# Kernel optimization log

Measured on AMD Instinct MI355X. Metric: run time of the kernel, lower is better.

The kernel has to match this reference:

```python
import jax, jax.numpy as jnp
import numpy as np

H = 8          # num_heads
T = 2          # num_edge_types
NEG_SLOPE = 0.2


def _edge_softmax(scores, dst, num_nodes):
    # softmax over incoming edges of each destination node, per head
    m = jax.ops.segment_max(scores, dst, num_segments=num_nodes)  # [N,H]
    e = jnp.exp(scores - m[dst])                                   # [E,H]
    s = jax.ops.segment_sum(e, dst, num_segments=num_nodes)        # [N,H]
    return e / s[dst]


def setup_inputs() -> dict:
    key = jax.random.key(0)
    ks = jax.random.split(key, 8)
    N, D, E = 50000, 128, 800000
    return {
        "x": jax.random.normal(ks[0], (N, D), dtype=jnp.float32),
        "w_u": jax.random.normal(ks[1], (H * T, D), dtype=jnp.float32) * (1.0 / np.sqrt(D)),
        "b_u": jax.random.normal(ks[2], (H * T,), dtype=jnp.float32) * 0.01,
        "w_v": jax.random.normal(ks[3], (H * T, D), dtype=jnp.float32) * (1.0 / np.sqrt(D)),
        "src_e0": jax.random.randint(ks[4], (E,), 0, N, dtype=jnp.int32),
        "dst_e0": jax.random.randint(ks[5], (E,), 0, N, dtype=jnp.int32),
        "src_e1": jax.random.randint(ks[6], (E,), 0, N, dtype=jnp.int32),
        "dst_e1": jax.random.randint(ks[7], (E,), 0, N, dtype=jnp.int32),
    }


def reference(x, w_u, b_u, w_v, src_e0, dst_e0, src_e1, dst_e1):
    N, D = x.shape
    head_dim = D // H
    scores_u = x @ w_u.T + b_u   # [N, H*T]
    scores_v = x @ w_v.T         # [N, H*T]
    xh = x.reshape(N, head_dim, H)  # matches torch reshape(-1, head_dim, num_heads)
    outs = [x]  # sep=True
    for t, (src, dst) in enumerate([(src_e0, dst_e0), (src_e1, dst_e1)]):
        u = scores_u[:, t * H:(t + 1) * H]
        v = scores_v[:, t * H:(t + 1) * H]
        s = u[src] + v[dst]                         # u_add_v -> [E,H]
        s = jnp.where(s >= 0, s, NEG_SLOPE * s)     # LeakyReLU(0.2)
        p = _edge_softmax(s, dst, N)                # [E,H]
        msg = xh[src] * p[:, None, :]               # u_mul_e -> [E,head_dim,H]
        agg = jax.ops.segment_sum(msg, dst, num_segments=N)  # [N,head_dim,H]
        outs.append(agg.reshape(N, D))
    return jnp.concatenate(outs, axis=-1)  # [N, D*(1+T)]
```

## Files before the change

### kernel.cpp

```cpp
#include <hip/hip_runtime.h>

#define NEG_SLOPE 0.2f
#define CHUNKP 2048
#define RSHIFT 11
#define RW     2048
#define MAXR   32

__device__ __forceinline__ ushort f2bf(float f) {
    union { float f; unsigned u; } c; c.f = f;
    unsigned u = c.u;
    return (ushort)((u + 0x7fffu + ((u >> 16) & 1u)) >> 16);
}

__global__ __launch_bounds__(256) void mega_kernel(
    const float* __restrict__ x, const float* __restrict__ wu,
    const float* __restrict__ bu, const float* __restrict__ wv,
    const int* __restrict__ s0, const int* __restrict__ d0,
    const int* __restrict__ s1, const int* __restrict__ d1,
    float* __restrict__ out, ushort* __restrict__ xbf,
    float* __restrict__ su, float* __restrict__ sv,
    int* __restrict__ gcur, unsigned* __restrict__ pairs,
    int N, int E, int nr, int cap, int convBlocks, int scoreBlocks, int ppset)
{
    __shared__ float wlds[32 * 129];
    __shared__ int lcnt[MAXR], gb[MAXR], lrun[MAXR];
    int tid = threadIdx.x;
    int bid = blockIdx.x;

    if (bid < convBlocks) {
        int i = bid * 256 + tid;
        if (i < N * 32) {
            float4 v = ((const float4*)x)[i];
            int n = i >> 5, q = i & 31;
            ((float4*)out)[(size_t)n * 96 + q] = v;
            ushort4 b;
            b.x = f2bf(v.x); b.y = f2bf(v.y); b.z = f2bf(v.z); b.w = f2bf(v.w);
            *(ushort4*)(xbf + (size_t)i * 4) = b;
        }
        return;
    }
    if (bid < convBlocks + scoreBlocks) {
        for (int i = tid; i < 4096; i += 256) {
            int o = i >> 7, k = i & 127;
            wlds[o * 129 + k] = (o < 16) ? wu[i] : wv[i - 2048];
        }
        __syncthreads();
        int o = tid & 15;
        int n = (bid - convBlocks) * 16 + (tid >> 4);
        if (n >= N) return;
        const float4* xr4 = (const float4*)(x + (size_t)n * 128);
        const float* wur = wlds + o * 129;
        const float* wvr = wlds + (16 + o) * 129;
        float au = 0.f, av = 0.f;
#pragma unroll
        for (int kk = 0; kk < 32; ++kk) {
            float4 xv = xr4[kk];
            int k = kk * 4;
            au = fmaf(xv.x, wur[k],     au);  av = fmaf(xv.x, wvr[k],     av);
            au = fmaf(xv.y, wur[k + 1], au);  av = fmaf(xv.y, wvr[k + 1], av);
            au = fmaf(xv.z, wur[k + 2], au);  av = fmaf(xv.z, wvr[k + 2], av);
            au = fmaf(xv.w, wur[k + 3], au);  av = fmaf(xv.w, wvr[k + 3], av);
        }
        su[n * 16 + o] = au + bu[o];
        sv[n * 16 + o] = av;
        return;
    }
    int pb = bid - convBlocks - scoreBlocks;
    int t = pb / ppset, c = pb % ppset;
    const int* ss = t ? s1 : s0;
    const int* dd = t ? d1 : d0;
    int beg = c * CHUNKP, end = min(E, beg + CHUNKP);
    if (tid < nr) lcnt[tid] = 0;
    __syncthreads();
    for (int e = beg + tid; e < end; e += 256)
        atomicAdd(&lcnt[dd[e] >> RSHIFT], 1);
    __syncthreads();
    if (tid < nr) {
        gb[tid] = atomicAdd(&gcur[t * MAXR + tid], lcnt[tid]);
        lrun[tid] = 0;
    }
    __syncthreads();
    unsigned* pt = pairs + (size_t)t * nr * cap;
    for (int e = beg + tid; e < end; e += 256) {
        int dst = dd[e], src = ss[e];
        int r = dst >> RSHIFT;
        int pos = atomicAdd(&lrun[r], 1);
        pt[(size_t)r * cap + gb[r] + pos] = ((unsigned)dst << 16) | (unsigned)src;
    }
}

__global__ __launch_bounds__(1024) void build_kernel(
    const unsigned* __restrict__ pairs, const int* __restrict__ gcur,
    int* __restrict__ off, ushort* __restrict__ bucket,
    int N, int E, int nr, int cap)
{
    __shared__ int hist[RW];
    __shared__ int lds[1024];
    int r = blockIdx.x, t = blockIdx.y, tid = threadIdx.x;
    int m = gcur[t * MAXR + r];
    int base = 0;
    if (tid < 32) {
        int v = (tid < r) ? gcur[t * MAXR + tid] : 0;
#pragma unroll
        for (int d = 1; d < 32; d <<= 1) v += __shfl_xor(v, d);
        if (tid == 0) lds[0] = v;
    }
    hist[tid] = 0; hist[tid + 1024] = 0;
    __syncthreads();
    base = lds[0];
    __syncthreads();
    const unsigned* p = pairs + ((size_t)t * nr + r) * cap;
    for (int i = tid; i < m; i += 1024)
        atomicAdd(&hist[(p[i] >> 16) & (RW - 1)], 1);
    __syncthreads();
    int h0 = hist[2 * tid], h1 = hist[2 * tid + 1];
    int tot = h0 + h1;
    lds[tid] = tot;
    __syncthreads();
    int incl = tot;
    for (int d = 1; d < 1024; d <<= 1) {
        int add = (tid >= d) ? lds[tid - d] : 0;
        __syncthreads();
        incl += add;
        lds[tid] = incl;
        __syncthreads();
    }
    int e0 = incl - tot, e1 = incl - tot + h0;
    int lo = r << RSHIFT;
    int* offt = off + (size_t)t * (N + 1);
    if (lo + 2 * tid < N)     offt[lo + 2 * tid]     = base + e0;
    if (lo + 2 * tid + 1 < N) offt[lo + 2 * tid + 1] = base + e1;
    hist[2 * tid] = e0; hist[2 * tid + 1] = e1;
    if (r == 0 && tid == 0) offt[N] = E;
    __syncthreads();
    ushort* bkt = bucket + (size_t)t * E + base;
    for (int i = tid; i < m; i += 1024) {
        unsigned v = p[i];
        int pos = atomicAdd(&hist[(v >> 16) & (RW - 1)], 1);
        bkt[pos] = (ushort)(v & 0xffffu);
    }
}

__global__ __launch_bounds__(256) void agg_kernel(
    const ushort* __restrict__ xbf, const float* __restrict__ su,
    const float* __restrict__ sv, const int* __restrict__ off,
    const ushort* __restrict__ bucket, float* __restrict__ out, int N, int E)
{
    __shared__ __align__(16) float evals[4][512];
    int t = blockIdx.y;
    int wid = threadIdx.x >> 6;
    int lane = threadIdx.x & 63;
    int n = blockIdx.x * 4 + wid;
    if (n >= N) return;
    const int* offt = off + (size_t)t * (N + 1);
    const ushort* bkt = bucket + (size_t)t * E;
    int beg = offt[n], end = offt[n + 1];
    int h = lane & 7;
    int e8 = lane >> 3;
    float vh = sv[n * 16 + t * 8 + h];
    float* ev = evals[wid];

    int hf = lane >> 5;
    int q = lane & 31;
    int j0 = q * 4;
    int hbase = (q & 1) * 4;
    float acc0 = 0.f, acc1 = 0.f, acc2 = 0.f, acc3 = 0.f;
    float l = 0.f;

    for (int cbeg = beg; cbeg < end; cbeg += 64) {
        int cnt = min(end - cbeg, 64);
        int gmax = (cnt + 7) >> 3;
        for (int g = 0; g < gmax; ++g) {
            int e = g * 8 + e8;
            bool valid = e < cnt;
            int srcv = 0;
            if (valid) srcv = bkt[cbeg + e];
            float s = su[srcv * 16 + t * 8 + h] + vh;
            s = (s >= 0.f) ? s : NEG_SLOPE * s;
            float eval = valid ? __expf(s) : 0.f;
            l += eval;
            ev[e * 8 + h] = eval;
        }
        int pairs2 = (cnt + 1) >> 1;
        for (int i2 = 0; i2 < pairs2; ++i2) {
            int eidx = i2 * 2 + hf;
            int srcv = 0;
            if (eidx < cnt) srcv = bkt[cbeg + eidx];
            float4 p4 = *(const float4*)(ev + eidx * 8 + hbase);
            uint2 u = *(const uint2*)(xbf + (size_t)srcv * 128 + j0);
            float x0 = __uint_as_float(u.x << 16);
            float x1 = __uint_as_float(u.x & 0xffff0000u);
            float x2 = __uint_as_float(u.y << 16);
            float x3 = __uint_as_float(u.y & 0xffff0000u);
            acc0 = fmaf(x0, p4.x, acc0);
            acc1 = fmaf(x1, p4.y, acc1);
            acc2 = fmaf(x2, p4.z, acc2);
            acc3 = fmaf(x3, p4.w, acc3);
        }
    }
    l += __shfl_xor(l, 8);
    l += __shfl_xor(l, 16);
    l += __shfl_xor(l, 32);
    float invl = (l > 0.f) ? (1.f / l) : 0.f;
    acc0 += __shfl_xor(acc0, 32);
    acc1 += __shfl_xor(acc1, 32);
    acc2 += __shfl_xor(acc2, 32);
    acc3 += __shfl_xor(acc3, 32);
    float i0 = __shfl(invl, hbase);
    float i1 = __shfl(invl, hbase + 1);
    float i2v = __shfl(invl, hbase + 2);
    float i3 = __shfl(invl, hbase + 3);
    if (hf == 0) {
        float4 r = make_float4(acc0 * i0, acc1 * i1, acc2 * i2v, acc3 * i3);
        *(float4*)(out + (size_t)n * 384 + 128 + (size_t)t * 128 + j0) = r;
    }
}

extern "C" void kernel_launch(void* const* d_in, const int* in_sizes, int n_in,
                              void* d_out, int out_size, void* d_ws, size_t ws_size,
                              hipStream_t stream)
{
    const float* x  = (const float*)d_in[0];
    const float* wu = (const float*)d_in[1];
    const float* bu = (const float*)d_in[2];
    const float* wv = (const float*)d_in[3];
    const int* s0 = (const int*)d_in[4];
    const int* d0 = (const int*)d_in[5];
    const int* s1 = (const int*)d_in[6];
    const int* d1 = (const int*)d_in[7];
    float* out = (float*)d_out;
    int N = in_sizes[0] / 128;
    int E = in_sizes[4];

    int nr = ((N - 1) >> RSHIFT) + 1;
    long long mean = (long long)RW * E / N;
    int cap = (int)(mean + mean / 4 + 2048);

    char* ws = (char*)d_ws;
    size_t o = 0;
    auto alloc = [&](size_t bytes) -> void* {
        void* p = ws + o;
        o = (o + bytes + 255) & ~(size_t)255;
        return p;
    };
    float* su       = (float*)alloc((size_t)N * 16 * 4);
    float* sv       = (float*)alloc((size_t)N * 16 * 4);
    int* gcur       = (int*)alloc((size_t)2 * MAXR * 4);
    int* off        = (int*)alloc((size_t)2 * (N + 1) * 4);
    unsigned* pairs = (unsigned*)alloc((size_t)2 * nr * cap * 4);
    ushort* bucket  = (ushort*)alloc((size_t)2 * E * 2);
    ushort* xbf     = (ushort*)alloc((size_t)N * 128 * 2);

    int convBlocks  = (N * 32 + 255) / 256;
    int scoreBlocks = (N + 15) / 16;
    int ppset       = (E + CHUNKP - 1) / CHUNKP;

    hipMemsetAsync(gcur, 0, (size_t)2 * MAXR * 4, stream);
    mega_kernel<<<convBlocks + scoreBlocks + 2 * ppset, 256, 0, stream>>>(
        x, wu, bu, wv, s0, d0, s1, d1, out, xbf, su, sv,
        gcur, pairs, N, E, nr, cap, convBlocks, scoreBlocks, ppset);
    build_kernel<<<dim3(nr, 2), 1024, 0, stream>>>(
        pairs, gcur, off, bucket, N, E, nr, cap);
    agg_kernel<<<dim3((N + 3) / 4, 2), 256, 0, stream>>>(
        xbf, su, sv, off, bucket, out, N, E);
}
```

Measured before the change: 273.4 us.

## Fuse all stages into one persistent cooperative kernel with grid syncs

Replaces the memset and the three separate kernel launches with a single cooperative persistent kernel. Grid-wide syncs separate the conversion/score, partition, CSR build and aggregation phases, and blocks loop over work items. The destination-range width shrinks from 2048 to 512 nodes, so there are more, smaller build items that fit 256-thread blocks, and per-block work is coarsened. This removes launch gaps and memset overhead. In exchange, grid barriers become a cost, and the persistent grid is sized by occupancy, which may limit parallelism in the aggregation phase.

New measurement: 1.064 ms. +289.0%, slower.

```diff
diff --git a/kernel.cpp b/kernel.cpp
--- a/kernel.cpp
+++ b/kernel.cpp
@@ -1,10 +1,12 @@
 #include <hip/hip_runtime.h>
+#include <hip/hip_cooperative_groups.h>
+
+namespace cg = cooperative_groups;
 
 #define NEG_SLOPE 0.2f
+#define RSHIFT 9
+#define RW     512
 #define CHUNKP 2048
-#define RSHIFT 11
-#define RW     2048
-#define MAXR   32
 
 __device__ __forceinline__ ushort f2bf(float f) {
     union { float f; unsigned u; } c; c.f = f;
@@ -12,7 +14,7 @@
     return (ushort)((u + 0x7fffu + ((u >> 16) & 1u)) >> 16);
 }
 
-__global__ __launch_bounds__(256) void mega_kernel(
+__global__ __launch_bounds__(256, 8) void fused_kernel(
     const float* __restrict__ x, const float* __restrict__ wu,
     const float* __restrict__ bu, const float* __restrict__ wv,
     const int* __restrict__ s0, const int* __restrict__ d0,
@@ -20,199 +22,208 @@
     float* __restrict__ out, ushort* __restrict__ xbf,
     float* __restrict__ su, float* __restrict__ sv,
     int* __restrict__ gcur, unsigned* __restrict__ pairs,
-    int N, int E, int nr, int cap, int convBlocks, int scoreBlocks, int ppset)
+    ushort* __restrict__ bucket, int* __restrict__ off,
+    int N, int E, int nr, int cap,
+    int convItems, int scoreItems, int partItems, int buildItems, int aggItems)
 {
-    __shared__ float wlds[32 * 129];
-    __shared__ int lcnt[MAXR], gb[MAXR], lrun[MAXR];
-    int tid = threadIdx.x;
-    int bid = blockIdx.x;
-
-    if (bid < convBlocks) {
-        int i = bid * 256 + tid;
-        if (i < N * 32) {
-            float4 v = ((const float4*)x)[i];
-            int n = i >> 5, q = i & 31;
-            ((float4*)out)[(size_t)n * 96 + q] = v;
-            ushort4 b;
-            b.x = f2bf(v.x); b.y = f2bf(v.y); b.z = f2bf(v.z); b.w = f2bf(v.w);
-            *(ushort4*)(xbf + (size_t)i * 4) = b;
-        }
-        return;
-    }
-    if (bid < convBlocks + scoreBlocks) {
-        for (int i = tid; i < 4096; i += 256) {
-            int o = i >> 7, k = i & 127;
-            wlds[o * 129 + k] = (o < 16) ? wu[i] : wv[i - 2048];
-        }
-        __syncthreads();
-        int o = tid & 15;
-        int n = (bid - convBlocks) * 16 + (tid >> 4);
-        if (n >= N) return;
-        const float4* xr4 = (const float4*)(x + (size_t)n * 128);
-        const float* wur = wlds + o * 129;
-        const float* wvr = wlds + (16 + o) * 129;
-        float au = 0.f, av = 0.f;
+    cg::grid_group grid = cg::this_grid();
+    __shared__ __align__(16) float smem[4224];
+    __shared__ int misc[8];
+    int* smi = (int*)smem;
+    const int tid = threadIdx.x;
+    const int nb = gridDim.x;
+    const int bid = blockIdx.x;
+
+    if (bid == 0) for (int i = tid; i < 2 * nr; i += 256) gcur[i] = 0;
+    int a1 = convItems + scoreItems;
+    for (int v = bid; v < a1; v += nb) {
+        if (v < convItems) {
+            int base = v * 2048 + tid;
 #pragma unroll
-        for (int kk = 0; kk < 32; ++kk) {
-            float4 xv = xr4[kk];
-            int k = kk * 4;
-            au = fmaf(xv.x, wur[k],     au);  av = fmaf(xv.x, wvr[k],     av);
-            au = fmaf(xv.y, wur[k + 1], au);  av = fmaf(xv.y, wvr[k + 1], av);
-            au = fmaf(xv.z, wur[k + 2], au);  av = fmaf(xv.z, wvr[k + 2], av);
-            au = fmaf(xv.w, wur[k + 3], au);  av = fmaf(xv.w, wvr[k + 3], av);
-        }
-        su[n * 16 + o] = au + bu[o];
-        sv[n * 16 + o] = av;
-        return;
-    }
-    int pb = bid - convBlocks - scoreBlocks;
-    int t = pb / ppset, c = pb % ppset;
-    const int* ss = t ? s1 : s0;
-    const int* dd = t ? d1 : d0;
-    int beg = c * CHUNKP, end = min(E, beg + CHUNKP);
-    if (tid < nr) lcnt[tid] = 0;
-    __syncthreads();
-    for (int e = beg + tid; e < end; e += 256)
-        atomicAdd(&lcnt[dd[e] >> RSHIFT], 1);
-    __syncthreads();
-    if (tid < nr) {
-        gb[tid] = atomicAdd(&gcur[t * MAXR + tid], lcnt[tid]);
-        lrun[tid] = 0;
-    }
-    __syncthreads();
-    unsigned* pt = pairs + (size_t)t * nr * cap;
-    for (int e = beg + tid; e < end; e += 256) {
-        int dst = dd[e], src = ss[e];
-        int r = dst >> RSHIFT;
-        int pos = atomicAdd(&lrun[r], 1);
-        pt[(size_t)r * cap + gb[r] + pos] = ((unsigned)dst << 16) | (unsigned)src;
-    }
-}
-
-__global__ __launch_bounds__(1024) void build_kernel(
-    const unsigned* __restrict__ pairs, const int* __restrict__ gcur,
-    int* __restrict__ off, ushort* __restrict__ bucket,
-    int N, int E, int nr, int cap)
-{
-    __shared__ int hist[RW];
-    __shared__ int lds[1024];
-    int r = blockIdx.x, t = blockIdx.y, tid = threadIdx.x;
-    int m = gcur[t * MAXR + r];
-    int base = 0;
-    if (tid < 32) {
-        int v = (tid < r) ? gcur[t * MAXR + tid] : 0;
+            for (int j = 0; j < 8; ++j) {
+                int i = base + j * 256;
+                if (i < N * 32) {
+                    float4 val = ((const float4*)x)[i];
+                    int n = i >> 5, q = i & 31;
+                    ((float4*)out)[(size_t)n * 96 + q] = val;
+                    ushort4 b;
+                    b.x = f2bf(val.x); b.y = f2bf(val.y);
+                    b.z = f2bf(val.z); b.w = f2bf(val.w);
+                    *(ushort4*)(xbf + (size_t)i * 4) = b;
+                }
+            }
+        } else {
+            int nbase = (v - convItems) * 128;
+            for (int i = tid; i < 4096; i += 256) {
+                int o = i >> 7, k = i & 127;
+                smem[o * 132 + k] = (o < 16) ? wu[i] : wv[i - 2048];
+            }
+            __syncthreads();
+            int o = tid & 15;
+            const float* wur = smem + o * 132;
+            const float* wvr = smem + (16 + o) * 132;
+            for (int sub = 0; sub < 8; ++sub) {
+                int n = nbase + sub * 16 + (tid >> 4);
+                if (n < N) {
+                    const float4* xr4 = (const float4*)(x + (size_t)n * 128);
+                    float au = 0.f, av = 0.f;
 #pragma unroll
-        for (int d = 1; d < 32; d <<= 1) v += __shfl_xor(v, d);
-        if (tid == 0) lds[0] = v;
-    }
-    hist[tid] = 0; hist[tid + 1024] = 0;
-    __syncthreads();
-    base = lds[0];
-    __syncthreads();
-    const unsigned* p = pairs + ((size_t)t * nr + r) * cap;
-    for (int i = tid; i < m; i += 1024)
-        atomicAdd(&hist[(p[i] >> 16) & (RW - 1)], 1);
-    __syncthreads();
-    int h0 = hist[2 * tid], h1 = hist[2 * tid + 1];
-    int tot = h0 + h1;
-    lds[tid] = tot;
-    __syncthreads();
-    int incl = tot;
-    for (int d = 1; d < 1024; d <<= 1) {
-        int add = (tid >= d) ? lds[tid - d] : 0;
-        __syncthreads();
-        incl += add;
-        lds[tid] = incl;
-        __syncthreads();
-    }
-    int e0 = incl - tot, e1 = incl - tot + h0;
-    int lo = r << RSHIFT;
-    int* offt = off + (size_t)t * (N + 1);
-    if (lo + 2 * tid < N)     offt[lo + 2 * tid]     = base + e0;
-    if (lo + 2 * tid + 1 < N) offt[lo + 2 * tid + 1] = base + e1;
-    hist[2 * tid] = e0; hist[2 * tid + 1] = e1;
-    if (r == 0 && tid == 0) offt[N] = E;
-    __syncthreads();
-    ushort* bkt = bucket + (size_t)t * E + base;
-    for (int i = tid; i < m; i += 1024) {
-        unsigned v = p[i];
-        int pos = atomicAdd(&hist[(v >> 16) & (RW - 1)], 1);
-        bkt[pos] = (ushort)(v & 0xffffu);
-    }
-}
-
-__global__ __launch_bounds__(256) void agg_kernel(
-    const ushort* __restrict__ xbf, const float* __restrict__ su,
-    const float* __restrict__ sv, const int* __restrict__ off,
-    const ushort* __restrict__ bucket, float* __restrict__ out, int N, int E)
-{
-    __shared__ __align__(16) float evals[4][512];
-    int t = blockIdx.y;
-    int wid = threadIdx.x >> 6;
-    int lane = threadIdx.x & 63;
-    int n = blockIdx.x * 4 + wid;
-    if (n >= N) return;
-    const int* offt = off + (size_t)t * (N + 1);
-    const ushort* bkt = bucket + (size_t)t * E;
-    int beg = offt[n], end = offt[n + 1];
-    int h = lane & 7;
-    int e8 = lane >> 3;
-    float vh = sv[n * 16 + t * 8 + h];
-    float* ev = evals[wid];
-
-    int hf = lane >> 5;
-    int q = lane & 31;
-    int j0 = q * 4;
-    int hbase = (q & 1) * 4;
-    float acc0 = 0.f, acc1 = 0.f, acc2 = 0.f, acc3 = 0.f;
-    float l = 0.f;
-
-    for (int cbeg = beg; cbeg < end; cbeg += 64) {
-        int cnt = min(end - cbeg, 64);
-        int gmax = (cnt + 7) >> 3;
-        for (int g = 0; g < gmax; ++g) {
-            int e = g * 8 + e8;
-            bool valid = e < cnt;
-            int srcv = 0;
-            if (valid) srcv = bkt[cbeg + e];
-            float s = su[srcv * 16 + t * 8 + h] + vh;
-            s = (s >= 0.f) ? s : NEG_SLOPE * s;
-            float eval = valid ? __expf(s) : 0.f;
-            l += eval;
-            ev[e * 8 + h] = eval;
-        }
-        int pairs2 = (cnt + 1) >> 1;
-        for (int i2 = 0; i2 < pairs2; ++i2) {
-            int eidx = i2 * 2 + hf;
-            int srcv = 0;
-            if (eidx < cnt) srcv = bkt[cbeg + eidx];
-            float4 p4 = *(const float4*)(ev + eidx * 8 + hbase);
-            uint2 u = *(const uint2*)(xbf + (size_t)srcv * 128 + j0);
-            float x0 = __uint_as_float(u.x << 16);
-            float x1 = __uint_as_float(u.x & 0xffff0000u);
-            float x2 = __uint_as_float(u.y << 16);
-            float x3 = __uint_as_float(u.y & 0xffff0000u);
-            acc0 = fmaf(x0, p4.x, acc0);
-            acc1 = fmaf(x1, p4.y, acc1);
-            acc2 = fmaf(x2, p4.z, acc2);
-            acc3 = fmaf(x3, p4.w, acc3);
-        }
-    }
-    l += __shfl_xor(l, 8);
-    l += __shfl_xor(l, 16);
-    l += __shfl_xor(l, 32);
-    float invl = (l > 0.f) ? (1.f / l) : 0.f;
-    acc0 += __shfl_xor(acc0, 32);
-    acc1 += __shfl_xor(acc1, 32);
-    acc2 += __shfl_xor(acc2, 32);
-    acc3 += __shfl_xor(acc3, 32);
-    float i0 = __shfl(invl, hbase);
-    float i1 = __shfl(invl, hbase + 1);
-    float i2v = __shfl(invl, hbase + 2);
-    float i3 = __shfl(invl, hbase + 3);
-    if (hf == 0) {
-        float4 r = make_float4(acc0 * i0, acc1 * i1, acc2 * i2v, acc3 * i3);
-        *(float4*)(out + (size_t)n * 384 + 128 + (size_t)t * 128 + j0) = r;
+                    for (int kk = 0; kk < 32; ++kk) {
+                        float4 xv = xr4[kk];
+                        float4 a4 = *(const float4*)(wur + kk * 4);
+                        float4 b4 = *(const float4*)(wvr + kk * 4);
+                        au = fmaf(xv.x, a4.x, au);  av = fmaf(xv.x, b4.x, av);
+                        au = fmaf(xv.y, a4.y, au);  av = fmaf(xv.y, b4.y, av);
+                        au = fmaf(xv.z, a4.z, au);  av = fmaf(xv.z, b4.z, av);
+                        au = fmaf(xv.w, a4.w, au);  av = fmaf(xv.w, b4.w, av);
+                    }
+                    su[n * 16 + o] = au + bu[o];
+                    sv[n * 16 + o] = av;
+                }
+            }
+            __syncthreads();
+        }
+    }
+    __threadfence();
+    grid.sync();
+
+    int ppset = partItems >> 1;
+    for (int v = bid; v < partItems; v += nb) {
+        int t = v / ppset, c = v % ppset;
+        const int* ss = t ? s1 : s0;
+        const int* dd = t ? d1 : d0;
+        int beg = c * CHUNKP, end = min(E, beg + CHUNKP);
+        int* lcnt = smi; int* gb = smi + 128; int* lrun = smi + 256;
+        if (tid < nr) lcnt[tid] = 0;
+        __syncthreads();
+        for (int e = beg + tid; e < end; e += 256)
+            atomicAdd(&lcnt[dd[e] >> RSHIFT], 1);
+        __syncthreads();
+        if (tid < nr) {
+            gb[tid] = atomicAdd(&gcur[t * nr + tid], lcnt[tid]);
+            lrun[tid] = 0;
+        }
+        __syncthreads();
+        unsigned* pt = pairs + (size_t)t * nr * cap;
+        for (int e = beg + tid; e < end; e += 256) {
+            int dst = dd[e], src = ss[e];
+            int r = dst >> RSHIFT;
+            int pos = atomicAdd(&lrun[r], 1);
+            pt[(size_t)r * cap + gb[r] + pos] = ((unsigned)dst << 16) | (unsigned)src;
+        }
+        __syncthreads();
+    }
+    __threadfence();
+    grid.sync();
+
+    for (int v = bid; v < buildItems; v += nb) {
+        int r = v % nr, t = v / nr;
+        int m = gcur[t * nr + r];
+        int s = (tid < r) ? gcur[t * nr + tid] : 0;
+#pragma unroll
+        for (int d = 1; d < 64; d <<= 1) s += __shfl_xor(s, d);
+        if ((tid & 63) == 0) misc[tid >> 6] = s;
+        int* hist = smi; int* scanb = smi + 512;
+        hist[2 * tid] = 0; hist[2 * tid + 1] = 0;
+        __syncthreads();
+        int base = misc[0] + misc[1] + misc[2] + misc[3];
+        const unsigned* p = pairs + ((size_t)t * nr + r) * cap;
+        for (int i = tid; i < m; i += 256)
+            atomicAdd(&hist[(p[i] >> 16) & (RW - 1)], 1);
+        __syncthreads();
+        int h0 = hist[2 * tid], h1 = hist[2 * tid + 1], tot = h0 + h1;
+        scanb[tid] = tot;
+        __syncthreads();
+        int incl = tot;
+        for (int d = 1; d < 256; d <<= 1) {
+            int add = (tid >= d) ? scanb[tid - d] : 0;
+            __syncthreads();
+            incl += add; scanb[tid] = incl;
+            __syncthreads();
+        }
+        int e0 = incl - tot, e1 = e0 + h0;
+        int lo = r << RSHIFT;
+        int* offt = off + (size_t)t * (N + 1);
+        if (lo + 2 * tid < N)     offt[lo + 2 * tid]     = base + e0;
+        if (lo + 2 * tid + 1 < N) offt[lo + 2 * tid + 1] = base + e1;
+        hist[2 * tid] = e0; hist[2 * tid + 1] = e1;
+        if (r == 0 && tid == 0) offt[N] = E;
+        __syncthreads();
+        ushort* bkt = bucket + (size_t)t * E + base;
+        for (int i = tid; i < m; i += 256) {
+            unsigned pv = p[i];
+            int pos = atomicAdd(&hist[(pv >> 16) & (RW - 1)], 1);
+            bkt[pos] = (ushort)(pv & 0xffffu);
+        }
+        __syncthreads();
+    }
+    __threadfence();
+    grid.sync();
+
+    {
+        int wid = tid >> 6, lane = tid & 63;
+        int h = lane & 7, e8 = lane >> 3;
+        int hf = lane >> 5, q = lane & 31;
+        int j0 = q * 4, hbase = (q & 1) * 4;
+        float* ev = smem + wid * 512;
+        for (int v = bid; v < aggItems; v += nb) {
+            int t = v & 1, gnode = v >> 1;
+            int n = gnode * 4 + wid;
+            if (n >= N) continue;
+            const int* offt = off + (size_t)t * (N + 1);
+            const ushort* bkt = bucket + (size_t)t * E;
+            int beg = offt[n], end = offt[n + 1];
+            float vh = sv[n * 16 + t * 8 + h];
+            float acc0 = 0.f, acc1 = 0.f, acc2 = 0.f, acc3 = 0.f;
+            float l = 0.f;
+            for (int cbeg = beg; cbeg < end; cbeg += 64) {
+                int cnt = min(end - cbeg, 64);
+                int gmax = (cnt + 7) >> 3;
+                for (int g = 0; g < gmax; ++g) {
+                    int e = g * 8 + e8;
+                    bool valid = e < cnt;
+                    int srcv = 0;
+                    if (valid) srcv = bkt[cbeg + e];
+                    float sc = su[srcv * 16 + t * 8 + h] + vh;
+                    sc = (sc >= 0.f) ? sc : NEG_SLOPE * sc;
+                    float eval = valid ? __expf(sc) : 0.f;
+                    l += eval;
+                    ev[e * 8 + h] = eval;
+                }
+                int pairs2 = (cnt + 1) >> 1;
+                for (int i2 = 0; i2 < pairs2; ++i2) {
+                    int eidx = i2 * 2 + hf;
+                    int srcv = 0;
+                    if (eidx < cnt) srcv = bkt[cbeg + eidx];
+                    float4 p4 = *(const float4*)(ev + eidx * 8 + hbase);
+                    uint2 u = *(const uint2*)(xbf + (size_t)srcv * 128 + j0);
+                    float x0 = __uint_as_float(u.x << 16);
+                    float x1 = __uint_as_float(u.x & 0xffff0000u);
+                    float x2 = __uint_as_float(u.y << 16);
+                    float x3 = __uint_as_float(u.y & 0xffff0000u);
+                    acc0 = fmaf(x0, p4.x, acc0);
+                    acc1 = fmaf(x1, p4.y, acc1);
+                    acc2 = fmaf(x2, p4.z, acc2);
+                    acc3 = fmaf(x3, p4.w, acc3);
+                }
+            }
+            l += __shfl_xor(l, 8);
+            l += __shfl_xor(l, 16);
+            l += __shfl_xor(l, 32);
+            float invl = (l > 0.f) ? (1.f / l) : 0.f;
+            acc0 += __shfl_xor(acc0, 32);
+            acc1 += __shfl_xor(acc1, 32);
+            acc2 += __shfl_xor(acc2, 32);
+            acc3 += __shfl_xor(acc3, 32);
+            float i0 = __shfl(invl, hbase);
+            float i1 = __shfl(invl, hbase + 1);
+            float i2v = __shfl(invl, hbase + 2);
+            float i3 = __shfl(invl, hbase + 3);
+            if (hf == 0) {
+                float4 r4 = make_float4(acc0 * i0, acc1 * i1, acc2 * i2v, acc3 * i3);
+                *(float4*)(out + (size_t)n * 384 + 128 + (size_t)t * 128 + j0) = r4;
+            }
+        }
     }
 }
 
@@ -234,7 +245,7 @@
 
     int nr = ((N - 1) >> RSHIFT) + 1;
     long long mean = (long long)RW * E / N;
-    int cap = (int)(mean + mean / 4 + 2048);
+    int cap = (int)(mean + mean / 4 + 1024);
 
     char* ws = (char*)d_ws;
     size_t o = 0;
@@ -245,22 +256,39 @@
     };
     float* su       = (float*)alloc((size_t)N * 16 * 4);
     float* sv       = (float*)alloc((size_t)N * 16 * 4);
-    int* gcur       = (int*)alloc((size_t)2 * MAXR * 4);
+    int* gcur       = (int*)alloc((size_t)2 * nr * 4);
     int* off        = (int*)alloc((size_t)2 * (N + 1) * 4);
     unsigned* pairs = (unsigned*)alloc((size_t)2 * nr * cap * 4);
     ushort* bucket  = (ushort*)alloc((size_t)2 * E * 2);
     ushort* xbf     = (ushort*)alloc((size_t)N * 128 * 2);
 
-    int convBlocks  = (N * 32 + 255) / 256;
-    int scoreBlocks = (N + 15) / 16;
-    int ppset       = (E + CHUNKP - 1) / CHUNKP;
-
-    hipMemsetAsync(gcur, 0, (size_t)2 * MAXR * 4, stream);
-    mega_kernel<<<convBlocks + scoreBlocks + 2 * ppset, 256, 0, stream>>>(
-        x, wu, bu, wv, s0, d0, s1, d1, out, xbf, su, sv,
-        gcur, pairs, N, E, nr, cap, convBlocks, scoreBlocks, ppset);
-    build_kernel<<<dim3(nr, 2), 1024, 0, stream>>>(
-        pairs, gcur, off, bucket, N, E, nr, cap);
-    agg_kernel<<<dim3((N + 3) / 4, 2), 256, 0, stream>>>(
-        xbf, su, sv, off, bucket, out, N, E);
+    int convItems  = (N * 32 + 2047) / 2048;
+    int scoreItems = (N + 127) / 128;
+    int partItems  = 2 * ((E + CHUNKP - 1) / CHUNKP);
+    int buildItems = 2 * nr;
+    int aggItems   = 2 * ((N + 3) / 4);
+
+    int dev = 0;
+    hipGetDevice(&dev);
+    int numCU = 0;
+    hipDeviceGetAttribute(&numCU, hipDeviceAttributeMultiprocessorCount, dev);
+    if (numCU <= 0) numCU = 256;
+    int maxB = 0;
+    hipOccupancyMaxActiveBlocksPerMultiprocessor(&maxB, fused_kernel, 256, 0);
+    if (maxB < 1) maxB = 1;
+    if (maxB > 8) maxB = 8;
+    int nb = numCU * maxB;
+    if (nb > 4096) nb = 4096;
+
+    void* args[] = {
+        (void*)&x, (void*)&wu, (void*)&bu, (void*)&wv,
+        (void*)&s0, (void*)&d0, (void*)&s1, (void*)&d1,
+        (void*)&out, (void*)&xbf, (void*)&su, (void*)&sv,
+        (void*)&gcur, (void*)&pairs, (void*)&bucket, (void*)&off,
+        (void*)&N, (void*)&E, (void*)&nr, (void*)&cap,
+        (void*)&convItems, (void*)&scoreItems, (void*)&partItems,
+        (void*)&buildItems, (void*)&aggItems
+    };
+    hipLaunchCooperativeKernel((const void*)fused_kernel, dim3(nb), dim3(256),
+                               args, 0, stream);
 }
```

## Fuse CSR build into aggregation using 64-node buckets sorted in LDS

Applied to the files above, without the earlier changes.

Destination regions shrink from 2048 nodes to 64 nodes. Each block of the new fused kernel now counting-sorts its region's packed (dst,src) pairs in shared memory and then aggregates the softmax-weighted messages directly. This removes the global offset and bucket arrays, one kernel launch, and the global round trip of the sorted source indices. In exchange, the partition kernel maintains far more per-chunk counters (up to 800, kept in reused LDS), and each wave processes 16 nodes in sequence. Per-region counts are clamped to a fixed capacity, so an unusually heavy region would silently drop edges.

After: 261.8 us. 4.3% less time.

```diff
diff --git a/kernel.cpp b/kernel.cpp
--- a/kernel.cpp
+++ b/kernel.cpp
@@ -1,10 +1,10 @@
 #include <hip/hip_runtime.h>
 
 #define NEG_SLOPE 0.2f
-#define CHUNKP 2048
-#define RSHIFT 11
-#define RW     2048
-#define MAXR   32
+#define RSHIFT 6
+#define RW     64
+#define MAXNR  800
+#define CHUNKP 8192
 
 __device__ __forceinline__ ushort f2bf(float f) {
     union { float f; unsigned u; } c; c.f = f;
@@ -23,7 +23,7 @@
     int N, int E, int nr, int cap, int convBlocks, int scoreBlocks, int ppset)
 {
     __shared__ float wlds[32 * 129];
-    __shared__ int lcnt[MAXR], gb[MAXR], lrun[MAXR];
+    int* smi = (int*)wlds;
     int tid = threadIdx.x;
     int bid = blockIdx.x;
 
@@ -70,14 +70,15 @@
     const int* ss = t ? s1 : s0;
     const int* dd = t ? d1 : d0;
     int beg = c * CHUNKP, end = min(E, beg + CHUNKP);
-    if (tid < nr) lcnt[tid] = 0;
+    int* lcnt = smi; int* gb = smi + MAXNR; int* lrun = smi + 2 * MAXNR;
+    for (int i = tid; i < nr; i += 256) lcnt[i] = 0;
     __syncthreads();
     for (int e = beg + tid; e < end; e += 256)
         atomicAdd(&lcnt[dd[e] >> RSHIFT], 1);
     __syncthreads();
-    if (tid < nr) {
-        gb[tid] = atomicAdd(&gcur[t * MAXR + tid], lcnt[tid]);
-        lrun[tid] = 0;
+    for (int i = tid; i < nr; i += 256) {
+        gb[i] = atomicAdd(&gcur[t * nr + i], lcnt[i]);
+        lrun[i] = 0;
     }
     __syncthreads();
     unsigned* pt = pairs + (size_t)t * nr * cap;
@@ -89,130 +90,103 @@
     }
 }
 
-__global__ __launch_bounds__(1024) void build_kernel(
-    const unsigned* __restrict__ pairs, const int* __restrict__ gcur,
-    int* __restrict__ off, ushort* __restrict__ bucket,
+__global__ __launch_bounds__(256, 8) void buildagg_kernel(
+    const ushort* __restrict__ xbf, const float* __restrict__ su,
+    const float* __restrict__ sv, const int* __restrict__ gcur,
+    const unsigned* __restrict__ pairs, float* __restrict__ out,
     int N, int E, int nr, int cap)
 {
-    __shared__ int hist[RW];
-    __shared__ int lds[1024];
+    __shared__ ushort srcs[1408];
+    __shared__ int offl[65];
+    __shared__ int cursor[64];
+    __shared__ __align__(16) float ev4[4][512];
     int r = blockIdx.x, t = blockIdx.y, tid = threadIdx.x;
-    int m = gcur[t * MAXR + r];
-    int base = 0;
-    if (tid < 32) {
-        int v = (tid < r) ? gcur[t * MAXR + tid] : 0;
+    int m = gcur[t * nr + r];
+    if (m > cap) m = cap;
+    const unsigned* p = pairs + ((size_t)t * nr + r) * cap;
+
+    if (tid < 64) cursor[tid] = 0;
+    __syncthreads();
+    for (int i = tid; i < m; i += 256)
+        atomicAdd(&cursor[(p[i] >> 16) & (RW - 1)], 1);
+    __syncthreads();
+    if (tid < 64) {
+        int v = cursor[tid];
+        int incl = v;
 #pragma unroll
-        for (int d = 1; d < 32; d <<= 1) v += __shfl_xor(v, d);
-        if (tid == 0) lds[0] = v;
-    }
-    hist[tid] = 0; hist[tid + 1024] = 0;
-    __syncthreads();
-    base = lds[0];
-    __syncthreads();
-    const unsigned* p = pairs + ((size_t)t * nr + r) * cap;
-    for (int i = tid; i < m; i += 1024)
-        atomicAdd(&hist[(p[i] >> 16) & (RW - 1)], 1);
-    __syncthreads();
-    int h0 = hist[2 * tid], h1 = hist[2 * tid + 1];
-    int tot = h0 + h1;
-    lds[tid] = tot;
-    __syncthreads();
-    int incl = tot;
-    for (int d = 1; d < 1024; d <<= 1) {
-        int add = (tid >= d) ? lds[tid - d] : 0;
-        __syncthreads();
-        incl += add;
-        lds[tid] = incl;
-        __syncthreads();
-    }
-    int e0 = incl - tot, e1 = incl - tot + h0;
-    int lo = r << RSHIFT;
-    int* offt = off + (size_t)t * (N + 1);
-    if (lo + 2 * tid < N)     offt[lo + 2 * tid]     = base + e0;
-    if (lo + 2 * tid + 1 < N) offt[lo + 2 * tid + 1] = base + e1;
-    hist[2 * tid] = e0; hist[2 * tid + 1] = e1;
-    if (r == 0 && tid == 0) offt[N] = E;
-    __syncthreads();
-    ushort* bkt = bucket + (size_t)t * E + base;
-    for (int i = tid; i < m; i += 1024) {
+        for (int d = 1; d < 64; d <<= 1) {
+            int o = __shfl(incl, tid - d);
+            if (tid >= d) incl += o;
+        }
+        offl[tid + 1] = incl;
+        if (tid == 0) offl[0] = 0;
+        cursor[tid] = incl - v;
+    }
+    __syncthreads();
+    for (int i = tid; i < m; i += 256) {
         unsigned v = p[i];
-        int pos = atomicAdd(&hist[(v >> 16) & (RW - 1)], 1);
-        bkt[pos] = (ushort)(v & 0xffffu);
-    }
-}
-
-__global__ __launch_bounds__(256) void agg_kernel(
-    const ushort* __restrict__ xbf, const float* __restrict__ su,
-    const float* __restrict__ sv, const int* __restrict__ off,
-    const ushort* __restrict__ bucket, float* __restrict__ out, int N, int E)
-{
-    __shared__ __align__(16) float evals[4][512];
-    int t = blockIdx.y;
-    int wid = threadIdx.x >> 6;
-    int lane = threadIdx.x & 63;
-    int n = blockIdx.x * 4 + wid;
-    if (n >= N) return;
-    const int* offt = off + (size_t)t * (N + 1);
-    const ushort* bkt = bucket + (size_t)t * E;
-    int beg = offt[n], end = offt[n + 1];
-    int h = lane & 7;
-    int e8 = lane >> 3;
-    float vh = sv[n * 16 + t * 8 + h];
-    float* ev = evals[wid];
-
-    int hf = lane >> 5;
-    int q = lane & 31;
-    int j0 = q * 4;
-    int hbase = (q & 1) * 4;
-    float acc0 = 0.f, acc1 = 0.f, acc2 = 0.f, acc3 = 0.f;
-    float l = 0.f;
-
-    for (int cbeg = beg; cbeg < end; cbeg += 64) {
-        int cnt = min(end - cbeg, 64);
-        int gmax = (cnt + 7) >> 3;
-        for (int g = 0; g < gmax; ++g) {
-            int e = g * 8 + e8;
-            bool valid = e < cnt;
-            int srcv = 0;
-            if (valid) srcv = bkt[cbeg + e];
-            float s = su[srcv * 16 + t * 8 + h] + vh;
-            s = (s >= 0.f) ? s : NEG_SLOPE * s;
-            float eval = valid ? __expf(s) : 0.f;
-            l += eval;
-            ev[e * 8 + h] = eval;
-        }
-        int pairs2 = (cnt + 1) >> 1;
-        for (int i2 = 0; i2 < pairs2; ++i2) {
-            int eidx = i2 * 2 + hf;
-            int srcv = 0;
-            if (eidx < cnt) srcv = bkt[cbeg + eidx];
-            float4 p4 = *(const float4*)(ev + eidx * 8 + hbase);
-            uint2 u = *(const uint2*)(xbf + (size_t)srcv * 128 + j0);
-            float x0 = __uint_as_float(u.x << 16);
-            float x1 = __uint_as_float(u.x & 0xffff0000u);
-            float x2 = __uint_as_float(u.y << 16);
-            float x3 = __uint_as_float(u.y & 0xffff0000u);
-            acc0 = fmaf(x0, p4.x, acc0);
-            acc1 = fmaf(x1, p4.y, acc1);
-            acc2 = fmaf(x2, p4.z, acc2);
-            acc3 = fmaf(x3, p4.w, acc3);
-        }
-    }
-    l += __shfl_xor(l, 8);
-    l += __shfl_xor(l, 16);
-    l += __shfl_xor(l, 32);
-    float invl = (l > 0.f) ? (1.f / l) : 0.f;
-    acc0 += __shfl_xor(acc0, 32);
-    acc1 += __shfl_xor(acc1, 32);
-    acc2 += __shfl_xor(acc2, 32);
-    acc3 += __shfl_xor(acc3, 32);
-    float i0 = __shfl(invl, hbase);
-    float i1 = __shfl(invl, hbase + 1);
-    float i2v = __shfl(invl, hbase + 2);
-    float i3 = __shfl(invl, hbase + 3);
-    if (hf == 0) {
-        float4 r = make_float4(acc0 * i0, acc1 * i1, acc2 * i2v, acc3 * i3);
-        *(float4*)(out + (size_t)n * 384 + 128 + (size_t)t * 128 + j0) = r;
+        int pos = atomicAdd(&cursor[(v >> 16) & (RW - 1)], 1);
+        srcs[pos] = (ushort)(v & 0xffffu);
+    }
+    __syncthreads();
+
+    int wid = tid >> 6, lane = tid & 63;
+    int h = lane & 7, e8 = lane >> 3;
+    int hf = lane >> 5, q = lane & 31;
+    int j0 = q * 4, hbase = (q & 1) * 4;
+    float* ev = ev4[wid];
+    for (int ln = wid; ln < RW; ln += 4) {
+        int n = (r << RSHIFT) + ln;
+        if (n >= N) break;
+        int beg = offl[ln], end = offl[ln + 1];
+        float vh = sv[n * 16 + t * 8 + h];
+        float acc0 = 0.f, acc1 = 0.f, acc2 = 0.f, acc3 = 0.f;
+        float l = 0.f;
+        for (int cbeg = beg; cbeg < end; cbeg += 64) {
+            int cnt = min(end - cbeg, 64);
+            int gmax = (cnt + 7) >> 3;
+            for (int g = 0; g < gmax; ++g) {
+                int e = g * 8 + e8;
+                bool valid = e < cnt;
+                int srcv = srcs[cbeg + (valid ? e : 0)];
+                float sc = su[srcv * 16 + t * 8 + h] + vh;
+                sc = (sc >= 0.f) ? sc : NEG_SLOPE * sc;
+                float ee = valid ? __expf(sc) : 0.f;
+                l += ee;
+                ev[e * 8 + h] = ee;
+            }
+            int pairs2 = (cnt + 1) >> 1;
+            for (int i2 = 0; i2 < pairs2; ++i2) {
+                int eidx = i2 * 2 + hf;
+                int srcv = srcs[cbeg + ((eidx < cnt) ? eidx : 0)];
+                float4 p4 = *(const float4*)(ev + eidx * 8 + hbase);
+                uint2 u = *(const uint2*)(xbf + (size_t)srcv * 128 + j0);
+                float x0 = __uint_as_float(u.x << 16);
+                float x1 = __uint_as_float(u.x & 0xffff0000u);
+                float x2 = __uint_as_float(u.y << 16);
+                float x3 = __uint_as_float(u.y & 0xffff0000u);
+                acc0 = fmaf(x0, p4.x, acc0);
+                acc1 = fmaf(x1, p4.y, acc1);
+                acc2 = fmaf(x2, p4.z, acc2);
+                acc3 = fmaf(x3, p4.w, acc3);
+            }
+        }
+        l += __shfl_xor(l, 8);
+        l += __shfl_xor(l, 16);
+        l += __shfl_xor(l, 32);
+        float invl = (l > 0.f) ? (1.f / l) : 0.f;
+        acc0 += __shfl_xor(acc0, 32);
+        acc1 += __shfl_xor(acc1, 32);
+        acc2 += __shfl_xor(acc2, 32);
+        acc3 += __shfl_xor(acc3, 32);
+        float i0 = __shfl(invl, hbase);
+        float i1 = __shfl(invl, hbase + 1);
+        float i2v = __shfl(invl, hbase + 2);
+        float i3 = __shfl(invl, hbase + 3);
+        if (hf == 0) {
+            float4 r4 = make_float4(acc0 * i0, acc1 * i1, acc2 * i2v, acc3 * i3);
+            *(float4*)(out + (size_t)n * 384 + 128 + (size_t)t * 128 + j0) = r4;
+        }
     }
 }
 
@@ -234,7 +208,7 @@
 
     int nr = ((N - 1) >> RSHIFT) + 1;
     long long mean = (long long)RW * E / N;
-    int cap = (int)(mean + mean / 4 + 2048);
+    int cap = (int)(mean + mean / 4 + 64);
 
     char* ws = (char*)d_ws;
     size_t o = 0;
@@ -245,22 +219,18 @@
     };
     float* su       = (float*)alloc((size_t)N * 16 * 4);
     float* sv       = (float*)alloc((size_t)N * 16 * 4);
-    int* gcur       = (int*)alloc((size_t)2 * MAXR * 4);
-    int* off        = (int*)alloc((size_t)2 * (N + 1) * 4);
+    int* gcur       = (int*)alloc((size_t)2 * nr * 4);
     unsigned* pairs = (unsigned*)alloc((size_t)2 * nr * cap * 4);
-    ushort* bucket  = (ushort*)alloc((size_t)2 * E * 2);
     ushort* xbf     = (ushort*)alloc((size_t)N * 128 * 2);
 
     int convBlocks  = (N * 32 + 255) / 256;
     int scoreBlocks = (N + 15) / 16;
     int ppset       = (E + CHUNKP - 1) / CHUNKP;
 
-    hipMemsetAsync(gcur, 0, (size_t)2 * MAXR * 4, stream);
+    hipMemsetAsync(gcur, 0, (size_t)2 * nr * 4, stream);
     mega_kernel<<<convBlocks + scoreBlocks + 2 * ppset, 256, 0, stream>>>(
         x, wu, bu, wv, s0, d0, s1, d1, out, xbf, su, sv,
         gcur, pairs, N, E, nr, cap, convBlocks, scoreBlocks, ppset);
-    build_kernel<<<dim3(nr, 2), 1024, 0, stream>>>(
-        pairs, gcur, off, bucket, N, E, nr, cap);
-    agg_kernel<<<dim3((N + 3) / 4, 2), 256, 0, stream>>>(
-        xbf, su, sv, off, bucket, out, N, E);
-}
+    buildagg_kernel<<<dim3(nr, 2), 256, 0, stream>>>(
+        xbf, su, sv, gcur, pairs, out, N, E, nr, cap);
+}
```
